# Kernel tuning notes

Measured on AMD Instinct MI355X. Metric: run time of the kernel, lower is better.

The kernel has to match this reference:

```python
import jax, jax.numpy as jnp
import numpy as np

B, S, D = 8, 4096, 256
SEG = 128  # per-entity segment length; num_entities = S // SEG = 32


def setup_inputs() -> dict:
    key = jax.random.key(0)
    k1, k2 = jax.random.split(key)
    hidden = jax.random.normal(k1, (B, S, D), dtype=jnp.float32)
    # additive attention mask: 0 = attend, finfo.min = masked. Use all-zeros (fully visible).
    hidden_mask = jnp.zeros((B, S, S), dtype=jnp.float32)
    # xavier_uniform_ for (emb_dim, d_model) = (256, 256)
    limit = float(np.sqrt(6.0 / (D + D)))
    w = jax.random.uniform(k2, (D, D), dtype=jnp.float32, minval=-limit, maxval=limit)
    b = jnp.zeros((1, D), dtype=jnp.float32)
    return {"hidden": hidden, "hidden_mask": hidden_mask, "w": w, "b": b, "seg_len": SEG}


def _forward(hidden, hidden_mask, w, b, seg_len):
    Bn, Sn, Dn = hidden.shape
    E = Sn // seg_len  # num_entities; equal-length ragged segments
    mask_val = jnp.finfo(hidden.dtype).min

    # [B, E, L, D] per-entity sequences (contiguous slices of hidden)
    seq = hidden.reshape(Bn, E, seg_len, Dn)

    # extract per-entity diagonal [L, L] blocks of the [S, S] mask
    m5 = hidden_mask.reshape(Bn, E, seg_len, E, seg_len)
    eidx = jnp.arange(E)
    blocks = m5[:, eidx, :, eidx, :]            # [E, B, L, L] (advanced indexing)
    blocks = jnp.transpose(blocks, (1, 0, 2, 3))  # [B, E, L, L]

    # original: if any row of an entity's mask is fully masked, unmask row 0
    row_all_masked = jnp.all(blocks == mask_val, axis=-1)   # [B, E, L]
    fix = jnp.any(row_all_masked, axis=(0, 2))              # [E]
    row0 = (jnp.arange(seg_len) == 0)                       # [L]
    blocks = jnp.where(fix[None, :, None, None] & row0[None, None, :, None],
                       jnp.zeros((), blocks.dtype), blocks)

    # attentive max pooling: scores = tanh(seq @ W^T + b) @ seq^T, masked softmax,
    # context = attn @ seq, then max over sequence positions.
    trsf = jnp.tanh(jnp.einsum('beld,md->belm', seq, w) + b[0])  # [B, E, L, M] (M == D)
    scores = jnp.einsum('belm,bekm->belk', trsf, seq)            # [B, E, L, L]
    attn = jax.nn.softmax(scores + blocks, axis=-1)
    ctx = jnp.einsum('belk,bekd->beld', attn, seq)               # [B, E, L, D]
    pooled = jnp.max(ctx, axis=2)                                # [B, E, D]

    # new_hidden_mask: 1 where position belongs to entity e, else 0
    pos_ent = jnp.arange(Sn) // seg_len                          # [S]
    new_mask = (pos_ent[None, :] == jnp.arange(E)[:, None]).astype(hidden_mask.dtype)
    new_mask = jnp.broadcast_to(new_mask[None], (Bn, E, Sn))
    return pooled, new_mask


def reference(hidden, hidden_mask, w, b, seg_len):
    return _forward(hidden, hidden_mask, w, b, seg_len)
```

## Files before the change

### kernel.cpp

```cpp
#include <hip/hip_runtime.h>

typedef __attribute__((ext_vector_type(8))) _Float16 f16x8;
typedef __attribute__((ext_vector_type(4))) _Float16 f16x4;
typedef __attribute__((ext_vector_type(4))) float f32x4;

#define LSTR 264
#define SS 4096
#define SD 256
#define SEG 128

__device__ __forceinline__ float fast_tanh(float x) {
    x = fminf(fmaxf(x, -15.f), 15.f);
    float ex = __expf(2.f * x);
    return (ex - 1.f) / (ex + 1.f);
}

extern "C" __global__ __launch_bounds__(256, 1)
void entity_tile_kernel(const float* __restrict__ hidden,
                        const float* __restrict__ mask,
                        const float* __restrict__ w,
                        const float* __restrict__ bias,
                        float* __restrict__ out)
{
    extern __shared__ _Float16 smem[];
    _Float16* s_trsf = smem;
    _Float16* s_seq  = smem + 128 * LSTR;

    const int bid  = blockIdx.x;
    const int b    = bid >> 5;
    const int e    = bid & 31;
    const int tid  = threadIdx.x;
    const int wv   = tid >> 6;
    const int lane = tid & 63;
    const int quad = lane >> 4;
    const int l15  = lane & 15;

    {
        const float4* g4 = (const float4*)(hidden + (size_t)bid * (SEG * SD));
        #pragma unroll
        for (int i = 0; i < 32; ++i) {
            int idx  = i * 256 + tid;
            int row  = idx >> 6;
            int col4 = (idx & 63) << 2;
            float4 v = g4[idx];
            f16x4 h = { (_Float16)v.x, (_Float16)v.y, (_Float16)v.z, (_Float16)v.w };
            *(f16x4*)&s_seq[row * LSTR + col4] = h;
        }
        float* nm = out + 65536 + (size_t)bid * 4096;
        #pragma unroll
        for (int i = 0; i < 4; ++i) {
            int idx = i * 256 + tid;
            float val = ((idx >> 5) == e) ? 1.0f : 0.0f;
            float4 q = {val, val, val, val};
            *(float4*)&nm[idx << 2] = q;
        }
    }

    float mraw[2][8][4];
    {
        const int lw = wv * 32;
        const size_t mbase = (((size_t)b * SS) + (size_t)e * SEG) * SS + (size_t)e * SEG;
        #pragma unroll
        for (int m2 = 0; m2 < 2; ++m2)
            #pragma unroll
            for (int r = 0; r < 4; ++r) {
                const int l = lw + m2 * 16 + quad * 4 + r;
                #pragma unroll
                for (int n = 0; n < 8; ++n)
                    mraw[m2][n][r] = mask[mbase + (size_t)l * SS + n * 16 + l15];
            }
    }
    __syncthreads();

    {
        const int wn0 = wv * 64;
        f16x8 wb[4][8];
        float bv[4];
        #pragma unroll
        for (int n = 0; n < 4; ++n) {
            const float* wrow = w + (size_t)(wn0 + n * 16 + l15) * SD;
            bv[n] = bias[wn0 + n * 16 + l15];
            #pragma unroll
            for (int k = 0; k < 8; ++k) {
                const float4* p = (const float4*)(wrow + k * 32 + quad * 8);
                float4 u0 = p[0], u1 = p[1];
                f16x8 v = { (_Float16)u0.x, (_Float16)u0.y, (_Float16)u0.z, (_Float16)u0.w,
                            (_Float16)u1.x, (_Float16)u1.y, (_Float16)u1.z, (_Float16)u1.w };
                wb[n][k] = v;
            }
        }
        const f32x4 fz = {0.f, 0.f, 0.f, 0.f};
        #pragma unroll
        for (int m = 0; m < 8; ++m) {
            f32x4 acc[4] = {fz, fz, fz, fz};
            #pragma unroll
            for (int k = 0; k < 8; ++k) {
                f16x8 a = *(const f16x8*)&s_seq[(m * 16 + l15) * LSTR + k * 32 + quad * 8];
                #pragma unroll
                for (int n = 0; n < 4; ++n)
                    acc[n] = __builtin_amdgcn_mfma_f32_16x16x32_f16(a, wb[n][k], acc[n], 0, 0, 0);
            }
            #pragma unroll
            for (int n = 0; n < 4; ++n)
                #pragma unroll
                for (int r = 0; r < 4; ++r)
                    s_trsf[(m * 16 + quad * 4 + r) * LSTR + wn0 + n * 16 + l15] =
                        (_Float16)fast_tanh(acc[n][r] + bv[n]);
        }
    }
    __syncthreads();

    {
        const int lw = wv * 32;
        f16x8 at[2][8];
        #pragma unroll
        for (int m2 = 0; m2 < 2; ++m2)
            #pragma unroll
            for (int k = 0; k < 8; ++k)
                at[m2][k] = *(const f16x8*)&s_trsf[(lw + m2 * 16 + l15) * LSTR + k * 32 + quad * 8];

        const f32x4 fz = {0.f, 0.f, 0.f, 0.f};
        f32x4 sacc[2][8];
        #pragma unroll
        for (int m2 = 0; m2 < 2; ++m2)
            #pragma unroll
            for (int n = 0; n < 8; ++n) sacc[m2][n] = fz;

        #pragma unroll
        for (int k = 0; k < 8; ++k) {
            #pragma unroll
            for (int n = 0; n < 8; ++n) {
                f16x8 bb = *(const f16x8*)&s_seq[(n * 16 + l15) * LSTR + k * 32 + quad * 8];
                sacc[0][n] = __builtin_amdgcn_mfma_f32_16x16x32_f16(at[0][k], bb, sacc[0][n], 0, 0, 0);
                sacc[1][n] = __builtin_amdgcn_mfma_f32_16x16x32_f16(at[1][k], bb, sacc[1][n], 0, 0, 0);
            }
        }

        #pragma unroll
        for (int m2 = 0; m2 < 2; ++m2) {
            #pragma unroll
            for (int r = 0; r < 4; ++r) {
                const int l = lw + m2 * 16 + quad * 4 + r;
                float mx = -3.4e38f;
                #pragma unroll
                for (int n = 0; n < 8; ++n) {
                    float sv = sacc[m2][n][r] + mraw[m2][n][r];
                    sacc[m2][n][r] = sv;
                    mx = fmaxf(mx, sv);
                }
                mx = fmaxf(mx, __shfl_xor(mx, 1, 64));
                mx = fmaxf(mx, __shfl_xor(mx, 2, 64));
                mx = fmaxf(mx, __shfl_xor(mx, 4, 64));
                mx = fmaxf(mx, __shfl_xor(mx, 8, 64));
                float sum = 0.f;
                #pragma unroll
                for (int n = 0; n < 8; ++n) {
                    float ev = __expf(sacc[m2][n][r] - mx);
                    sacc[m2][n][r] = ev;
                    sum += ev;
                }
                sum += __shfl_xor(sum, 1, 64);
                sum += __shfl_xor(sum, 2, 64);
                sum += __shfl_xor(sum, 4, 64);
                sum += __shfl_xor(sum, 8, 64);
                float inv = 1.f / sum;
                #pragma unroll
                for (int n = 0; n < 8; ++n)
                    s_trsf[(size_t)l * LSTR + n * 16 + l15] = (_Float16)(sacc[m2][n][r] * inv);
            }
        }
    }
    __syncthreads();

    {
        f16x8 af[8][4];
        #pragma unroll
        for (int m = 0; m < 8; ++m)
            #pragma unroll
            for (int k = 0; k < 4; ++k)
                af[m][k] = *(const f16x8*)&s_trsf[(m * 16 + l15) * LSTR + k * 32 + quad * 8];

        const int wn0 = wv * 64;
        const f32x4 fz = {0.f, 0.f, 0.f, 0.f};
        #pragma unroll
        for (int n = 0; n < 4; ++n) {
            f16x8 bfr[4];
            #pragma unroll
            for (int k = 0; k < 4; ++k) {
                f16x8 t;
                #pragma unroll
                for (int j = 0; j < 8; ++j)
                    t[j] = s_seq[(k * 32 + quad * 8 + j) * LSTR + wn0 + n * 16 + l15];
                bfr[k] = t;
            }
            f32x4 a[8];
            #pragma unroll
            for (int m = 0; m < 8; ++m) a[m] = fz;
            #pragma unroll
            for (int k = 0; k < 4; ++k)
                #pragma unroll
                for (int m = 0; m < 8; ++m)
                    a[m] = __builtin_amdgcn_mfma_f32_16x16x32_f16(af[m][k], bfr[k], a[m], 0, 0, 0);

            float cm = -3.4e38f;
            #pragma unroll
            for (int m = 0; m < 8; ++m)
                #pragma unroll
                for (int r = 0; r < 4; ++r)
                    cm = fmaxf(cm, a[m][r]);
            cm = fmaxf(cm, __shfl_xor(cm, 16, 64));
            cm = fmaxf(cm, __shfl_xor(cm, 32, 64));
            if (quad == 0)
                out[bid * 256 + wn0 + n * 16 + l15] = cm;
        }
    }
}

extern "C" void kernel_launch(void* const* d_in, const int* in_sizes, int n_in,
                              void* d_out, int out_size, void* d_ws, size_t ws_size,
                              hipStream_t stream) {
    const float* hidden = (const float*)d_in[0];
    const float* mask   = (const float*)d_in[1];
    const float* w      = (const float*)d_in[2];
    const float* bias   = (const float*)d_in[3];
    float* out = (float*)d_out;

    const size_t lds_bytes = (size_t)(2 * 128 * LSTR) * sizeof(_Float16);
    hipFuncSetAttribute(reinterpret_cast<const void*>(entity_tile_kernel),
                        hipFuncAttributeMaxDynamicSharedMemorySize, (int)lds_bytes);
    hipLaunchKernelGGL(entity_tile_kernel, dim3(256), dim3(256), lds_bytes, stream,
                       hidden, mask, w, bias, out);
}
```

Baseline: 614.1 us.

## Use 8 waves per block and split work across twice as many wavefronts

```diff
diff --git a/kernel.cpp b/kernel.cpp
--- a/kernel.cpp
+++ b/kernel.cpp
@@ -15,7 +15,7 @@
     return (ex - 1.f) / (ex + 1.f);
 }
 
-extern "C" __global__ __launch_bounds__(256, 1)
+extern "C" __global__ __launch_bounds__(512, 2)
 void entity_tile_kernel(const float* __restrict__ hidden,
                         const float* __restrict__ mask,
                         const float* __restrict__ w,
@@ -38,8 +38,8 @@
     {
         const float4* g4 = (const float4*)(hidden + (size_t)bid * (SEG * SD));
         #pragma unroll
-        for (int i = 0; i < 32; ++i) {
-            int idx  = i * 256 + tid;
+        for (int i = 0; i < 16; ++i) {
+            int idx  = i * 512 + tid;
             int row  = idx >> 6;
             int col4 = (idx & 63) << 2;
             float4 v = g4[idx];
@@ -48,126 +48,121 @@
         }
         float* nm = out + 65536 + (size_t)bid * 4096;
         #pragma unroll
-        for (int i = 0; i < 4; ++i) {
-            int idx = i * 256 + tid;
+        for (int i = 0; i < 2; ++i) {
+            int idx = i * 512 + tid;
             float val = ((idx >> 5) == e) ? 1.0f : 0.0f;
             float4 q = {val, val, val, val};
             *(float4*)&nm[idx << 2] = q;
         }
     }
 
-    float mraw[2][8][4];
-    {
-        const int lw = wv * 32;
+    float mraw[8][4];
+    {
+        const int lw = wv * 16;
         const size_t mbase = (((size_t)b * SS) + (size_t)e * SEG) * SS + (size_t)e * SEG;
         #pragma unroll
-        for (int m2 = 0; m2 < 2; ++m2)
-            #pragma unroll
-            for (int r = 0; r < 4; ++r) {
-                const int l = lw + m2 * 16 + quad * 4 + r;
-                #pragma unroll
-                for (int n = 0; n < 8; ++n)
-                    mraw[m2][n][r] = mask[mbase + (size_t)l * SS + n * 16 + l15];
-            }
+        for (int r = 0; r < 4; ++r) {
+            const int l = lw + quad * 4 + r;
+            #pragma unroll
+            for (int n = 0; n < 8; ++n)
+                mraw[n][r] = mask[mbase + (size_t)l * SS + n * 16 + l15];
+        }
     }
     __syncthreads();
 
     {
-        const int wn0 = wv * 64;
-        f16x8 wb[4][8];
-        float bv[4];
-        #pragma unroll
-        for (int n = 0; n < 4; ++n) {
-            const float* wrow = w + (size_t)(wn0 + n * 16 + l15) * SD;
-            bv[n] = bias[wn0 + n * 16 + l15];
+        const int wn0 = wv * 32;
+        f16x8 wb[2][8];
+        float bv[2];
+        #pragma unroll
+        for (int nn = 0; nn < 2; ++nn) {
+            const float* wrow = w + (size_t)(wn0 + nn * 16 + l15) * SD;
+            bv[nn] = bias[wn0 + nn * 16 + l15];
             #pragma unroll
             for (int k = 0; k < 8; ++k) {
                 const float4* p = (const float4*)(wrow + k * 32 + quad * 8);
                 float4 u0 = p[0], u1 = p[1];
                 f16x8 v = { (_Float16)u0.x, (_Float16)u0.y, (_Float16)u0.z, (_Float16)u0.w,
                             (_Float16)u1.x, (_Float16)u1.y, (_Float16)u1.z, (_Float16)u1.w };
-                wb[n][k] = v;
+                wb[nn][k] = v;
             }
         }
         const f32x4 fz = {0.f, 0.f, 0.f, 0.f};
         #pragma unroll
-        for (int m = 0; m < 8; ++m) {
-            f32x4 acc[4] = {fz, fz, fz, fz};
+        for (int m2 = 0; m2 < 4; ++m2) {
+            f32x4 acc[2][2] = {{fz, fz}, {fz, fz}};
             #pragma unroll
             for (int k = 0; k < 8; ++k) {
-                f16x8 a = *(const f16x8*)&s_seq[(m * 16 + l15) * LSTR + k * 32 + quad * 8];
-                #pragma unroll
-                for (int n = 0; n < 4; ++n)
-                    acc[n] = __builtin_amdgcn_mfma_f32_16x16x32_f16(a, wb[n][k], acc[n], 0, 0, 0);
-            }
-            #pragma unroll
-            for (int n = 0; n < 4; ++n)
-                #pragma unroll
-                for (int r = 0; r < 4; ++r)
-                    s_trsf[(m * 16 + quad * 4 + r) * LSTR + wn0 + n * 16 + l15] =
-                        (_Float16)fast_tanh(acc[n][r] + bv[n]);
+                f16x8 a0 = *(const f16x8*)&s_seq[(m2 * 32 +      l15) * LSTR + k * 32 + quad * 8];
+                f16x8 a1 = *(const f16x8*)&s_seq[(m2 * 32 + 16 + l15) * LSTR + k * 32 + quad * 8];
+                #pragma unroll
+                for (int nn = 0; nn < 2; ++nn) {
+                    acc[0][nn] = __builtin_amdgcn_mfma_f32_16x16x32_f16(a0, wb[nn][k], acc[0][nn], 0, 0, 0);
+                    acc[1][nn] = __builtin_amdgcn_mfma_f32_16x16x32_f16(a1, wb[nn][k], acc[1][nn], 0, 0, 0);
+                }
+            }
+            #pragma unroll
+            for (int h = 0; h < 2; ++h)
+                #pragma unroll
+                for (int nn = 0; nn < 2; ++nn)
+                    #pragma unroll
+                    for (int r = 0; r < 4; ++r)
+                        s_trsf[(m2 * 32 + h * 16 + quad * 4 + r) * LSTR + wn0 + nn * 16 + l15] =
+                            (_Float16)fast_tanh(acc[h][nn][r] + bv[nn]);
         }
     }
     __syncthreads();
 
     {
-        const int lw = wv * 32;
-        f16x8 at[2][8];
-        #pragma unroll
-        for (int m2 = 0; m2 < 2; ++m2)
-            #pragma unroll
-            for (int k = 0; k < 8; ++k)
-                at[m2][k] = *(const f16x8*)&s_trsf[(lw + m2 * 16 + l15) * LSTR + k * 32 + quad * 8];
+        const int lw = wv * 16;
+        f16x8 at[8];
+        #pragma unroll
+        for (int k = 0; k < 8; ++k)
+            at[k] = *(const f16x8*)&s_trsf[(lw + l15) * LSTR + k * 32 + quad * 8];
 
         const f32x4 fz = {0.f, 0.f, 0.f, 0.f};
-        f32x4 sacc[2][8];
-        #pragma unroll
-        for (int m2 = 0; m2 < 2; ++m2)
-            #pragma unroll
-            for (int n = 0; n < 8; ++n) sacc[m2][n] = fz;
+        f32x4 sacc[8];
+        #pragma unroll
+        for (int n = 0; n < 8; ++n) sacc[n] = fz;
 
         #pragma unroll
         for (int k = 0; k < 8; ++k) {
             #pragma unroll
             for (int n = 0; n < 8; ++n) {
                 f16x8 bb = *(const f16x8*)&s_seq[(n * 16 + l15) * LSTR + k * 32 + quad * 8];
-                sacc[0][n] = __builtin_amdgcn_mfma_f32_16x16x32_f16(at[0][k], bb, sacc[0][n], 0, 0, 0);
-                sacc[1][n] = __builtin_amdgcn_mfma_f32_16x16x32_f16(at[1][k], bb, sacc[1][n], 0, 0, 0);
-            }
-        }
-
-        #pragma unroll
-        for (int m2 = 0; m2 < 2; ++m2) {
-            #pragma unroll
-            for (int r = 0; r < 4; ++r) {
-                const int l = lw + m2 * 16 + quad * 4 + r;
-                float mx = -3.4e38f;
-                #pragma unroll
-                for (int n = 0; n < 8; ++n) {
-                    float sv = sacc[m2][n][r] + mraw[m2][n][r];
-                    sacc[m2][n][r] = sv;
-                    mx = fmaxf(mx, sv);
-                }
-                mx = fmaxf(mx, __shfl_xor(mx, 1, 64));
-                mx = fmaxf(mx, __shfl_xor(mx, 2, 64));
-                mx = fmaxf(mx, __shfl_xor(mx, 4, 64));
-                mx = fmaxf(mx, __shfl_xor(mx, 8, 64));
-                float sum = 0.f;
-                #pragma unroll
-                for (int n = 0; n < 8; ++n) {
-                    float ev = __expf(sacc[m2][n][r] - mx);
-                    sacc[m2][n][r] = ev;
-                    sum += ev;
-                }
-                sum += __shfl_xor(sum, 1, 64);
-                sum += __shfl_xor(sum, 2, 64);
-                sum += __shfl_xor(sum, 4, 64);
-                sum += __shfl_xor(sum, 8, 64);
-                float inv = 1.f / sum;
-                #pragma unroll
-                for (int n = 0; n < 8; ++n)
-                    s_trsf[(size_t)l * LSTR + n * 16 + l15] = (_Float16)(sacc[m2][n][r] * inv);
-            }
+                sacc[n] = __builtin_amdgcn_mfma_f32_16x16x32_f16(at[k], bb, sacc[n], 0, 0, 0);
+            }
+        }
+
+        #pragma unroll
+        for (int r = 0; r < 4; ++r) {
+            const int l = lw + quad * 4 + r;
+            float mx = -3.4e38f;
+            #pragma unroll
+            for (int n = 0; n < 8; ++n) {
+                float sv = sacc[n][r] + mraw[n][r];
+                sacc[n][r] = sv;
+                mx = fmaxf(mx, sv);
+            }
+            mx = fmaxf(mx, __shfl_xor(mx, 1, 64));
+            mx = fmaxf(mx, __shfl_xor(mx, 2, 64));
+            mx = fmaxf(mx, __shfl_xor(mx, 4, 64));
+            mx = fmaxf(mx, __shfl_xor(mx, 8, 64));
+            float sum = 0.f;
+            #pragma unroll
+            for (int n = 0; n < 8; ++n) {
+                float ev = __expf(sacc[n][r] - mx);
+                sacc[n][r] = ev;
+                sum += ev;
+            }
+            sum += __shfl_xor(sum, 1, 64);
+            sum += __shfl_xor(sum, 2, 64);
+            sum += __shfl_xor(sum, 4, 64);
+            sum += __shfl_xor(sum, 8, 64);
+            float inv = 1.f / sum;
+            #pragma unroll
+            for (int n = 0; n < 8; ++n)
+                s_trsf[(size_t)l * LSTR + n * 16 + l15] = (_Float16)(sacc[n][r] * inv);
         }
     }
     __syncthreads();
@@ -180,17 +175,17 @@
             for (int k = 0; k < 4; ++k)
                 af[m][k] = *(const f16x8*)&s_trsf[(m * 16 + l15) * LSTR + k * 32 + quad * 8];
 
-        const int wn0 = wv * 64;
+        const int wn0 = wv * 32;
         const f32x4 fz = {0.f, 0.f, 0.f, 0.f};
         #pragma unroll
-        for (int n = 0; n < 4; ++n) {
+        for (int nn = 0; nn < 2; ++nn) {
             f16x8 bfr[4];
             #pragma unroll
             for (int k = 0; k < 4; ++k) {
                 f16x8 t;
                 #pragma unroll
                 for (int j = 0; j < 8; ++j)
-                    t[j] = s_seq[(k * 32 + quad * 8 + j) * LSTR + wn0 + n * 16 + l15];
+                    t[j] = s_seq[(k * 32 + quad * 8 + j) * LSTR + wn0 + nn * 16 + l15];
                 bfr[k] = t;
             }
             f32x4 a[8];
@@ -211,7 +206,7 @@
             cm = fmaxf(cm, __shfl_xor(cm, 16, 64));
             cm = fmaxf(cm, __shfl_xor(cm, 32, 64));
             if (quad == 0)
-                out[bid * 256 + wn0 + n * 16 + l15] = cm;
+                out[bid * 256 + wn0 + nn * 16 + l15] = cm;
         }
     }
 }
@@ -228,6 +223,6 @@
     const size_t lds_bytes = (size_t)(2 * 128 * LSTR) * sizeof(_Float16);
     hipFuncSetAttribute(reinterpret_cast<const void*>(entity_tile_kernel),
                         hipFuncAttributeMaxDynamicSharedMemorySize, (int)lds_bytes);
-    hipLaunchKernelGGL(entity_tile_kernel, dim3(256), dim3(256), lds_bytes, stream,
+    hipLaunchKernelGGL(entity_tile_kernel, dim3(256), dim3(512), lds_bytes, stream,
                        hidden, mask, w, bias, out);
 }
```

Result: no change. 610.9 us (-0.5%).
